# Kernel optimization log

Measured on AMD Instinct MI355X. Metric: run time of the kernel, lower is better.

The kernel has to match this reference:

```python
import jax, jax.numpy as jnp
import numpy as np

SUBSTEPS = 2  # fixed Tsit5 substeps per observation interval (replaces diffrax adaptive PID control)
# Tsit5 Butcher tableau (same stage math as diffrax.Tsit5)
C2, C3, C4, C5, C6 = 0.161, 0.327, 0.9, 0.9800255409045097, 1.0
A21 = 0.161
A31, A32 = -0.008480655492356989, 0.335480655492357
A41, A42, A43 = 2.8971530571054935, -6.359448489975075, 4.3622954328695815
A51, A52, A53, A54 = 5.325864828439257, -11.748883564062828, 7.4955393428898365, -0.09249506636175525
A61, A62, A63, A64, A65 = 5.86145544294642, -12.92096931784711, 8.159367898576159, -0.071584973281401, -0.028269050394068383
B1, B2, B3, B4, B5, B6 = 0.09646076681806523, 0.01, 0.4798896504144996, 1.379008574103742, -3.290069515436081, 2.324710524099774


def setup_inputs() -> dict:
    key = jax.random.key(0)
    ks = jax.random.split(key, 12)
    B, N, D_IN, H, ST, SW, OW, D_OUT = 128, 64, 32, 128, 16, 256, 256, 16

    def lin(k, o, i):
        return jax.random.normal(k, (o, i), jnp.float32) / np.sqrt(i).astype(np.float32)

    # strictly increasing timestamps with small intervals
    dts = jax.random.uniform(ks[0], (B, N), jnp.float32) * 0.05 + 0.01
    ts_batch = jnp.cumsum(dts, axis=1)
    X_batch = jax.random.normal(ks[1], (B, N, D_IN), jnp.float32)
    Static_batch = jax.random.normal(ks[2], (B, ST), jnp.float32)
    return dict(
        ts_batch=ts_batch, X_batch=X_batch, Static_batch=Static_batch,
        ode_w0=lin(ks[3], SW, 1 + H), ode_b0=jnp.zeros(SW, jnp.float32),
        ode_w1=lin(ks[4], SW, SW), ode_b1=jnp.zeros(SW, jnp.float32),
        ode_w2=lin(ks[5], H, SW), ode_b2=jnp.zeros(H, jnp.float32),
        ode_scale=jnp.array(1.0, jnp.float32),
        rnn_wh=lin(ks[6], H, H), rnn_wx=lin(ks[7], H, D_IN), rnn_bx=jnp.zeros(H, jnp.float32),
        inj_w=lin(ks[8], H, H + ST), inj_b=jnp.zeros(H, jnp.float32),
        out_w0=lin(ks[9], OW, H), out_b0=jnp.zeros(OW, jnp.float32),
        out_w1=lin(ks[10], OW, OW), out_b1=jnp.zeros(OW, jnp.float32),
        out_w2=lin(ks[11], D_OUT, OW), out_b2=jnp.zeros(D_OUT, jnp.float32),
    )


def reference(ts_batch, X_batch, Static_batch,
              ode_w0, ode_b0, ode_w1, ode_b1, ode_w2, ode_b2, ode_scale,
              rnn_wh, rnn_wx, rnn_bx, inj_w, inj_b,
              out_w0, out_b0, out_w1, out_b1, out_w2, out_b2):
    def f(t, h):  # vector field: t (B,), h (B,H)
        z = jnp.concatenate([t[:, None], h], axis=-1)
        z = jax.nn.silu(z @ ode_w0.T + ode_b0)
        z = jax.nn.silu(z @ ode_w1.T + ode_b1)
        return ode_scale * jnp.tanh(z @ ode_w2.T + ode_b2)

    def tsit5_step(t, dt, y):  # one Tsit5 step, batched over B
        d = dt[:, None]
        k1 = f(t, y)
        k2 = f(t + C2 * dt, y + d * (A21 * k1))
        k3 = f(t + C3 * dt, y + d * (A31 * k1 + A32 * k2))
        k4 = f(t + C4 * dt, y + d * (A41 * k1 + A42 * k2 + A43 * k3))
        k5 = f(t + C5 * dt, y + d * (A51 * k1 + A52 * k2 + A53 * k3 + A54 * k4))
        k6 = f(t + C6 * dt, y + d * (A61 * k1 + A62 * k2 + A63 * k3 + A64 * k4 + A65 * k5))
        return y + d * (B1 * k1 + B2 * k2 + B3 * k3 + B4 * k4 + B5 * k5 + B6 * k6)

    def ode_solve(t0, t1, y):  # fixed-substep Tsit5 integration from t0 to t1 (per-batch times)
        dt = (t1 - t0) / SUBSTEPS
        def body(yc, i):
            t = t0 + i.astype(t0.dtype) * dt
            return tsit5_step(t, dt, yc), None
        y, _ = jax.lax.scan(body, y, jnp.arange(SUBSTEPS))
        return y

    def rnn(h_prime, x):
        return jnp.tanh(h_prime @ rnn_wh.T + x @ rnn_wx.T + rnn_bx)

    # h0: rnn_cell(zeros, x0) -> inject static -> tanh
    h0 = jnp.tanh(X_batch[:, 0] @ rnn_wx.T + rnn_bx)  # hidden_linear(0) == 0
    h0 = jnp.tanh(jnp.concatenate([h0, Static_batch], axis=-1) @ inj_w.T + inj_b)

    xs = (ts_batch[:, :-1].T, ts_batch[:, 1:].T, jnp.swapaxes(X_batch[:, 1:], 0, 1))
    def step(h, inp):
        tp, tn, x = inp
        hp = ode_solve(tp, tn, h)
        return rnn(hp, x), None
    hN, _ = jax.lax.scan(step, h0, xs)

    z = jnp.tanh(hN @ out_w0.T + out_b0)
    z = jnp.tanh(z @ out_w1.T + out_b1)
    return z @ out_w2.T + out_b2  # (B, output_dim)
```

## Files before the change

### kernel.cpp

```cpp
#include <hip/hip_runtime.h>

typedef _Float16 f16;
typedef _Float16 f16x4 __attribute__((ext_vector_type(4)));
typedef _Float16 f16x8 __attribute__((ext_vector_type(8)));
typedef float f32x4 __attribute__((ext_vector_type(4)));

#define MFMA16(a, b, c) __builtin_amdgcn_mfma_f32_16x16x32_f16((a), (b), (c), 0, 0, 0)

#define A21f 0.161f
#define A31f (-0.008480655492356989f)
#define A32f 0.335480655492357f
#define A41f 2.8971530571054935f
#define A42f (-6.359448489975075f)
#define A43f 4.3622954328695815f
#define A51f 5.325864828439257f
#define A52f (-11.748883564062828f)
#define A53f 7.4955393428898365f
#define A54f (-0.09249506636175525f)
#define A61f 5.86145544294642f
#define A62f (-12.92096931784711f)
#define A63f 8.159367898576159f
#define A64f (-0.071584973281401f)
#define A65f (-0.028269050394068383f)
#define B1f 0.09646076681806523f
#define B2f 0.01f
#define B3f 0.4798896504144996f
#define B4f 1.379008574103742f
#define B5f (-3.290069515436081f)
#define B6f 2.324710524099774f
#define C2f 0.161f
#define C3f 0.327f
#define C4f 0.9f
#define C5f 0.9800255409045097f
#define C6f 1.0f

#define LDS_Y   0
#define LDS_Z1  4096
#define LDS_Z2  12288
#define LDS_X   20480
#define LDS_TS  21504
#define LDS_WH  25600
#define LDS_TOT 58368

__device__ __forceinline__ float tanh_fast(float x) {
  return 2.0f * __builtin_amdgcn_rcpf(1.0f + __expf(-2.0f * x)) - 1.0f;
}
__device__ __forceinline__ float siluf(float x) {
  return x * __builtin_amdgcn_rcpf(1.0f + __expf(-x));
}

__global__ __launch_bounds__(512, 2)
void ode_rnn_kernel(const float* __restrict__ ts, const float* __restrict__ Xg,
                    const float* __restrict__ Sg,
                    const float* __restrict__ w0g, const float* __restrict__ b0g,
                    const float* __restrict__ w1g, const float* __restrict__ b1g,
                    const float* __restrict__ w2g, const float* __restrict__ b2g,
                    const float* __restrict__ scaleg,
                    const float* __restrict__ whg, const float* __restrict__ wxg,
                    const float* __restrict__ bxg,
                    const float* __restrict__ injwg, const float* __restrict__ injbg,
                    const float* __restrict__ ow0g, const float* __restrict__ ob0g,
                    const float* __restrict__ ow1g, const float* __restrict__ ob1g,
                    const float* __restrict__ ow2g, const float* __restrict__ ob2g,
                    float* __restrict__ outg) {
  const int t  = threadIdx.x;
  const int w  = t >> 6;
  const int l  = t & 63;
  const int lr = l & 15;
  const int lg = l >> 4;
  const int rb = blockIdx.x * 16;
  const int c1 = w * 32;
  const int c3 = w * 16;

  __shared__ __align__(16) unsigned char lds[LDS_TOT];

  const int ard = l * 16;
  const int whrd = LDS_WH + lg * 2048 + w * 256 + lr * 16;
  const int awb = (lg >> 1) * 256 + lr * 16 + (lg & 1) * 8;

  for (int e = t; e < 16 * 64; e += 512) {
    *(float*)(lds + LDS_TS + e * 4) = ts[(size_t)(rb + (e >> 6)) * 64 + (e & 63)];
  }
  for (int e = t; e < 128 * 128; e += 512) {
    int c = e >> 7, kk = e & 127;
    *(f16*)(lds + LDS_WH + ((kk >> 3) * 128 + c) * 16 + (kk & 7) * 2) = (f16)whg[e];
  }
  {
    int r = t >> 5, d = t & 31;
    *(f16*)(lds + LDS_X + (d >> 3) * 256 + r * 16 + (d & 7) * 2) =
        (f16)Xg[(size_t)(rb + r) * 2048 + d];
  }
  if (t < 256) {
    int r = t >> 4, c = t & 15;
    *(f16*)(lds + LDS_Z1 + 4096 + (c >> 3) * 256 + r * 16 + (c & 7) * 2) =
        (f16)Sg[(size_t)(rb + r) * 16 + c];
    *(f16*)(lds + LDS_Z1 + 4608 + (c >> 3) * 256 + r * 16 + (c & 7) * 2) = (f16)0.0f;
  }

  f32x4 b0q[2], b1q[2];
  float w0c0[2][4];
  #pragma unroll
  for (int nt = 0; nt < 2; ++nt) {
    b0q[nt] = *(const f32x4*)(b0g + c1 + nt * 16 + lg * 4);
    b1q[nt] = *(const f32x4*)(b1g + c1 + nt * 16 + lg * 4);
    #pragma unroll
    for (int r = 0; r < 4; ++r)
      w0c0[nt][r] = w0g[(size_t)(c1 + nt * 16 + lg * 4 + r) * 129];
  }
  const f32x4 b2q = *(const f32x4*)(b2g + c3 + lg * 4);
  const f32x4 bxq = *(const f32x4*)(bxg + c3 + lg * 4);
  const float scalev = scaleg[0];

  auto ldfrag = [](const float* p) {
    f16x8 v;
    #pragma unroll
    for (int j = 0; j < 8; ++j) v[j] = (f16)p[j];
    return v;
  };

  f16x8 W0f[4][2];
  #pragma unroll
  for (int kt = 0; kt < 4; ++kt)
    #pragma unroll
    for (int nt = 0; nt < 2; ++nt)
      W0f[kt][nt] = ldfrag(w0g + (size_t)(c1 + nt * 16 + lr) * 129 + 1 + kt * 32 + lg * 8);

  f16x8 W1f[8][2];
  #pragma unroll
  for (int kt = 0; kt < 8; ++kt)
    #pragma unroll
    for (int nt = 0; nt < 2; ++nt)
      W1f[kt][nt] = ldfrag(w1g + (size_t)(c1 + nt * 16 + lr) * 256 + kt * 32 + lg * 8);

  f16x8 W2f[8];
  #pragma unroll
  for (int kt = 0; kt < 8; ++kt)
    W2f[kt] = ldfrag(w2g + (size_t)(c3 + lr) * 256 + kt * 32 + lg * 8);

  f16x8 WXf = ldfrag(wxg + (size_t)(c3 + lr) * 32 + lg * 8);

  __syncthreads();

  float y[4];
  float tpv, dvv;

  auto writeY = [&](const float* yv) {
    f16x4 p;
    #pragma unroll
    for (int r = 0; r < 4; ++r) p[r] = (f16)yv[r];
    *(f16x4*)(lds + LDS_Y + w * 512 + awb) = p;
  };

  {
    f16x8 xa = *(const f16x8*)(lds + LDS_X + ard);
    f32x4 acc = {};
    acc = MFMA16(WXf, xa, acc);
    f16x4 p;
    #pragma unroll
    for (int r = 0; r < 4; ++r) p[r] = (f16)tanh_fast(acc[r] + bxq[r]);
    *(f16x4*)(lds + LDS_Z1 + w * 512 + awb) = p;
  }
  __syncthreads();
  {
    f16x8 af[5];
    #pragma unroll
    for (int kt = 0; kt < 5; ++kt) af[kt] = *(const f16x8*)(lds + LDS_Z1 + ard + kt * 1024);
    f32x4 acc = {};
    #pragma unroll
    for (int kt = 0; kt < 5; ++kt) {
      f16x8 bf;
      #pragma unroll
      for (int j = 0; j < 8; ++j) {
        int k = kt * 32 + lg * 8 + j;
        bf[j] = (k < 144) ? (f16)injwg[(size_t)(c3 + lr) * 144 + k] : (f16)0.0f;
      }
      acc = MFMA16(bf, af[kt], acc);
    }
    const f32x4 ibq = *(const f32x4*)(injbg + c3 + lg * 4);
    #pragma unroll
    for (int r = 0; r < 4; ++r) y[r] = tanh_fast(acc[r] + ibq[r]);
  }
  writeY(y);
  __syncthreads();

  auto feval = [&](float sc, float* ko) {
    f16x8 af[8];
    #pragma unroll
    for (int kt = 0; kt < 4; ++kt) af[kt] = *(const f16x8*)(lds + LDS_Y + ard + kt * 1024);
    f32x4 a1[2] = {}, a1b[2] = {};
    __builtin_amdgcn_s_setprio(1);
    #pragma unroll
    for (int kt = 0; kt < 2; ++kt)
      #pragma unroll
      for (int nt = 0; nt < 2; ++nt) {
        a1[nt]  = MFMA16(W0f[kt][nt],     af[kt],     a1[nt]);
        a1b[nt] = MFMA16(W0f[kt + 2][nt], af[kt + 2], a1b[nt]);
      }
    __builtin_amdgcn_s_setprio(0);
    const float tr = tpv + sc * dvv;
    #pragma unroll
    for (int nt = 0; nt < 2; ++nt) {
      f16x4 p;
      #pragma unroll
      for (int r = 0; r < 4; ++r)
        p[r] = (f16)siluf(a1[nt][r] + a1b[nt][r] + tr * w0c0[nt][r] + b0q[nt][r]);
      *(f16x4*)(lds + LDS_Z1 + w * 1024 + nt * 512 + awb) = p;
    }
    __syncthreads();
    #pragma unroll
    for (int kt = 0; kt < 8; ++kt) af[kt] = *(const f16x8*)(lds + LDS_Z1 + ard + kt * 1024);
    f32x4 a2[2] = {}, a2b[2] = {};
    __builtin_amdgcn_s_setprio(1);
    #pragma unroll
    for (int kt = 0; kt < 4; ++kt)
      #pragma unroll
      for (int nt = 0; nt < 2; ++nt) {
        a2[nt]  = MFMA16(W1f[kt][nt],     af[kt],     a2[nt]);
        a2b[nt] = MFMA16(W1f[kt + 4][nt], af[kt + 4], a2b[nt]);
      }
    __builtin_amdgcn_s_setprio(0);
    #pragma unroll
    for (int nt = 0; nt < 2; ++nt) {
      f16x4 p;
      #pragma unroll
      for (int r = 0; r < 4; ++r)
        p[r] = (f16)siluf(a2[nt][r] + a2b[nt][r] + b1q[nt][r]);
      *(f16x4*)(lds + LDS_Z2 + w * 1024 + nt * 512 + awb) = p;
    }
    __syncthreads();
    #pragma unroll
    for (int kt = 0; kt < 8; ++kt) af[kt] = *(const f16x8*)(lds + LDS_Z2 + ard + kt * 1024);
    f32x4 a3 = {}, a3b = {}, a3c = {}, a3d = {};
    __builtin_amdgcn_s_setprio(1);
    #pragma unroll
    for (int kt = 0; kt < 2; ++kt) {
      a3  = MFMA16(W2f[kt],     af[kt],     a3);
      a3b = MFMA16(W2f[kt + 2], af[kt + 2], a3b);
      a3c = MFMA16(W2f[kt + 4], af[kt + 4], a3c);
      a3d = MFMA16(W2f[kt + 6], af[kt + 6], a3d);
    }
    __builtin_amdgcn_s_setprio(0);
    #pragma unroll
    for (int r = 0; r < 4; ++r)
      ko[r] = scalev * tanh_fast(((a3[r] + a3b[r]) + (a3c[r] + a3d[r])) + b2q[r]);
  };

  #pragma unroll 1
  for (int n = 0; n < 63; ++n) {
    {
      float tp = *(const float*)(lds + LDS_TS + (lr * 64 + n) * 4);
      float tn = *(const float*)(lds + LDS_TS + (lr * 64 + n + 1) * 4);
      tpv = tp;
      dvv = (tn - tp) * 0.5f;
    }
    {
      int r = t >> 5, d = t & 31;
      *(f16*)(lds + LDS_X + (d >> 3) * 256 + r * 16 + (d & 7) * 2) =
          (f16)Xg[(size_t)(rb + r) * 2048 + (size_t)(n + 1) * 32 + d];
    }

    #pragma unroll 1
    for (int s = 0; s < 2; ++s) {
      float k1v[4], k2v[4], k3v[4], k4v[4], k5v[4], k6v[4], yt[4];
      float sf = (float)s;
      feval(sf, k1v);
      #pragma unroll
      for (int i = 0; i < 4; ++i) yt[i] = y[i] + dvv * (A21f * k1v[i]);
      writeY(yt); __syncthreads();
      feval(sf + C2f, k2v);
      #pragma unroll
      for (int i = 0; i < 4; ++i) yt[i] = y[i] + dvv * (A31f * k1v[i] + A32f * k2v[i]);
      writeY(yt); __syncthreads();
      feval(sf + C3f, k3v);
      #pragma unroll
      for (int i = 0; i < 4; ++i) yt[i] = y[i] + dvv * (A41f * k1v[i] + A42f * k2v[i] + A43f * k3v[i]);
      writeY(yt); __syncthreads();
      feval(sf + C4f, k4v);
      #pragma unroll
      for (int i = 0; i < 4; ++i) yt[i] = y[i] + dvv * (A51f * k1v[i] + A52f * k2v[i] + A53f * k3v[i] + A54f * k4v[i]);
      writeY(yt); __syncthreads();
      feval(sf + C5f, k5v);
      #pragma unroll
      for (int i = 0; i < 4; ++i) yt[i] = y[i] + dvv * (A61f * k1v[i] + A62f * k2v[i] + A63f * k3v[i] + A64f * k4v[i] + A65f * k5v[i]);
      writeY(yt); __syncthreads();
      feval(sf + C6f, k6v);
      #pragma unroll
      for (int i = 0; i < 4; ++i)
        y[i] += dvv * (B1f * k1v[i] + B2f * k2v[i] + B3f * k3v[i] + B4f * k4v[i] + B5f * k5v[i] + B6f * k6v[i]);
      writeY(y); __syncthreads();
    }

    {
      f16x8 ha[4];
      #pragma unroll
      for (int kt = 0; kt < 4; ++kt) ha[kt] = *(const f16x8*)(lds + LDS_Y + ard + kt * 1024);
      f16x8 xa = *(const f16x8*)(lds + LDS_X + ard);
      f32x4 acc = {}, accb = {};
      __builtin_amdgcn_s_setprio(1);
      #pragma unroll
      for (int kt = 0; kt < 2; ++kt) {
        f16x8 bf  = *(const f16x8*)(lds + whrd + kt * 8192);
        f16x8 bf2 = *(const f16x8*)(lds + whrd + (kt + 2) * 8192);
        acc  = MFMA16(bf,  ha[kt],     acc);
        accb = MFMA16(bf2, ha[kt + 2], accb);
      }
      acc = MFMA16(WXf, xa, acc);
      __builtin_amdgcn_s_setprio(0);
      #pragma unroll
      for (int r = 0; r < 4; ++r) y[r] = tanh_fast(acc[r] + accb[r] + bxq[r]);
      writeY(y);
      __syncthreads();
    }
  }

  auto ldfrag2 = [](const float* p) {
    f16x8 v;
    #pragma unroll
    for (int j = 0; j < 8; ++j) v[j] = (f16)p[j];
    return v;
  };
  {
    f16x8 ha[4];
    #pragma unroll
    for (int kt = 0; kt < 4; ++kt) ha[kt] = *(const f16x8*)(lds + LDS_Y + ard + kt * 1024);
    f32x4 acc[2] = {};
    #pragma unroll
    for (int kt = 0; kt < 4; ++kt)
      #pragma unroll
      for (int nt = 0; nt < 2; ++nt) {
        f16x8 bf = ldfrag2(ow0g + (size_t)(c1 + nt * 16 + lr) * 128 + kt * 32 + lg * 8);
        acc[nt] = MFMA16(bf, ha[kt], acc[nt]);
      }
    #pragma unroll
    for (int nt = 0; nt < 2; ++nt) {
      const f32x4 bb = *(const f32x4*)(ob0g + c1 + nt * 16 + lg * 4);
      f16x4 p;
      #pragma unroll
      for (int r = 0; r < 4; ++r) p[r] = (f16)tanh_fast(acc[nt][r] + bb[r]);
      *(f16x4*)(lds + LDS_Z1 + w * 1024 + nt * 512 + awb) = p;
    }
  }
  __syncthreads();
  {
    f16x8 za[8];
    #pragma unroll
    for (int kt = 0; kt < 8; ++kt) za[kt] = *(const f16x8*)(lds + LDS_Z1 + ard + kt * 1024);
    f32x4 acc[2] = {};
    #pragma unroll
    for (int kt = 0; kt < 8; ++kt)
      #pragma unroll
      for (int nt = 0; nt < 2; ++nt) {
        f16x8 bf = ldfrag2(ow1g + (size_t)(c1 + nt * 16 + lr) * 256 + kt * 32 + lg * 8);
        acc[nt] = MFMA16(bf, za[kt], acc[nt]);
      }
    #pragma unroll
    for (int nt = 0; nt < 2; ++nt) {
      const f32x4 bb = *(const f32x4*)(ob1g + c1 + nt * 16 + lg * 4);
      f16x4 p;
      #pragma unroll
      for (int r = 0; r < 4; ++r) p[r] = (f16)tanh_fast(acc[nt][r] + bb[r]);
      *(f16x4*)(lds + LDS_Z2 + w * 1024 + nt * 512 + awb) = p;
    }
  }
  __syncthreads();
  if (w == 0) {
    f16x8 za[8];
    #pragma unroll
    for (int kt = 0; kt < 8; ++kt) za[kt] = *(const f16x8*)(lds + LDS_Z2 + ard + kt * 1024);
    f32x4 acc = {};
    #pragma unroll
    for (int kt = 0; kt < 8; ++kt) {
      f16x8 bf = ldfrag2(ow2g + (size_t)lr * 256 + kt * 32 + lg * 8);
      acc = MFMA16(bf, za[kt], acc);
    }
    const f32x4 bb = *(const f32x4*)(ob2g + lg * 4);
    f32x4 vout;
    #pragma unroll
    for (int r = 0; r < 4; ++r) vout[r] = acc[r] + bb[r];
    *(f32x4*)(outg + (size_t)(rb + lr) * 16 + lg * 4) = vout;
  }
}

extern "C" void kernel_launch(void* const* d_in, const int* in_sizes, int n_in,
                              void* d_out, int out_size, void* d_ws, size_t ws_size,
                              hipStream_t stream) {
  (void)in_sizes; (void)n_in; (void)d_ws; (void)ws_size; (void)out_size;
  ode_rnn_kernel<<<dim3(8), dim3(512), 0, stream>>>(
      (const float*)d_in[0],  (const float*)d_in[1],  (const float*)d_in[2],
      (const float*)d_in[3],  (const float*)d_in[4],  (const float*)d_in[5],
      (const float*)d_in[6],  (const float*)d_in[7],  (const float*)d_in[8],
      (const float*)d_in[9],  (const float*)d_in[10], (const float*)d_in[11],
      (const float*)d_in[12], (const float*)d_in[13], (const float*)d_in[14],
      (const float*)d_in[15], (const float*)d_in[16], (const float*)d_in[17],
      (const float*)d_in[18], (const float*)d_in[19], (const float*)d_in[20],
      (float*)d_out);
}
```

Measured before the change: 1.163 ms.

## Use LDS-only barriers, double-buffer X prefetch, packed f16 conversion, reorder MFMAs

Replaces __syncthreads in the hot ODE loop with a barrier that waits only on lgkmcnt, so the global load of the next X row is no longer drained at every barrier. X is now double-buffered in LDS, and the next row is loaded into a register one step ahead, then written after the substeps. The f16 packing uses cvt_pkrtz (round toward zero rather than round-to-nearest), which slightly changes numerics. MFMA accumulation order is restructured per output tile.

```diff
diff --git a/kernel.cpp b/kernel.cpp
--- a/kernel.cpp
+++ b/kernel.cpp
@@ -1,9 +1,9 @@
 #include <hip/hip_runtime.h>
 
 typedef _Float16 f16;
-typedef _Float16 f16x4 __attribute__((ext_vector_type(4)));
 typedef _Float16 f16x8 __attribute__((ext_vector_type(8)));
 typedef float f32x4 __attribute__((ext_vector_type(4)));
+typedef unsigned u32x2 __attribute__((ext_vector_type(2)));
 
 #define MFMA16(a, b, c) __builtin_amdgcn_mfma_f32_16x16x32_f16((a), (b), (c), 0, 0, 0)
 
@@ -37,16 +37,25 @@
 #define LDS_Y   0
 #define LDS_Z1  4096
 #define LDS_Z2  12288
-#define LDS_X   20480
-#define LDS_TS  21504
-#define LDS_WH  25600
-#define LDS_TOT 58368
+#define LDS_X0  20480
+#define LDS_X1  21504
+#define LDS_TS  22528
+#define LDS_WH  26624
+#define LDS_TOT 59392
 
 __device__ __forceinline__ float tanh_fast(float x) {
   return 2.0f * __builtin_amdgcn_rcpf(1.0f + __expf(-2.0f * x)) - 1.0f;
 }
 __device__ __forceinline__ float siluf(float x) {
   return x * __builtin_amdgcn_rcpf(1.0f + __expf(-x));
+}
+__device__ __forceinline__ unsigned pk2(float a, float b) {
+  return __builtin_bit_cast(unsigned, __builtin_amdgcn_cvt_pkrtz(a, b));
+}
+__device__ __forceinline__ void bar_lds() {
+  asm volatile("s_waitcnt lgkmcnt(0)" ::: "memory");
+  __builtin_amdgcn_s_barrier();
+  __builtin_amdgcn_sched_barrier(0);
 }
 
 __global__ __launch_bounds__(512, 2)
@@ -74,9 +83,11 @@
 
   __shared__ __align__(16) unsigned char lds[LDS_TOT];
 
-  const int ard = l * 16;
+  const int ard  = l * 16;
   const int whrd = LDS_WH + lg * 2048 + w * 256 + lr * 16;
-  const int awb = (lg >> 1) * 256 + lr * 16 + (lg & 1) * 8;
+  const int awb  = (lg >> 1) * 256 + lr * 16 + (lg & 1) * 8;
+  const int xr = t >> 5, xd = t & 31;
+  const int xso = (xd >> 3) * 256 + xr * 16 + (xd & 7) * 2;
 
   for (int e = t; e < 16 * 64; e += 512) {
     *(float*)(lds + LDS_TS + e * 4) = ts[(size_t)(rb + (e >> 6)) * 64 + (e & 63)];
@@ -86,9 +97,9 @@
     *(f16*)(lds + LDS_WH + ((kk >> 3) * 128 + c) * 16 + (kk & 7) * 2) = (f16)whg[e];
   }
   {
-    int r = t >> 5, d = t & 31;
-    *(f16*)(lds + LDS_X + (d >> 3) * 256 + r * 16 + (d & 7) * 2) =
-        (f16)Xg[(size_t)(rb + r) * 2048 + d];
+    size_t base = (size_t)(rb + xr) * 2048 + xd;
+    *(f16*)(lds + LDS_X0 + xso) = (f16)Xg[base];
+    *(f16*)(lds + LDS_X1 + xso) = (f16)Xg[base + 32];
   }
   if (t < 256) {
     int r = t >> 4, c = t & 15;
@@ -145,20 +156,17 @@
   float tpv, dvv;
 
   auto writeY = [&](const float* yv) {
-    f16x4 p;
-    #pragma unroll
-    for (int r = 0; r < 4; ++r) p[r] = (f16)yv[r];
-    *(f16x4*)(lds + LDS_Y + w * 512 + awb) = p;
+    u32x2 p = { pk2(yv[0], yv[1]), pk2(yv[2], yv[3]) };
+    *(u32x2*)(lds + LDS_Y + w * 512 + awb) = p;
   };
 
   {
-    f16x8 xa = *(const f16x8*)(lds + LDS_X + ard);
+    f16x8 xa = *(const f16x8*)(lds + LDS_X0 + ard);
     f32x4 acc = {};
     acc = MFMA16(WXf, xa, acc);
-    f16x4 p;
-    #pragma unroll
-    for (int r = 0; r < 4; ++r) p[r] = (f16)tanh_fast(acc[r] + bxq[r]);
-    *(f16x4*)(lds + LDS_Z1 + w * 512 + awb) = p;
+    u32x2 p = { pk2(tanh_fast(acc[0] + bxq[0]), tanh_fast(acc[1] + bxq[1])),
+                pk2(tanh_fast(acc[2] + bxq[2]), tanh_fast(acc[3] + bxq[3])) };
+    *(u32x2*)(lds + LDS_Z1 + w * 512 + awb) = p;
   }
   __syncthreads();
   {
@@ -187,47 +195,59 @@
     f16x8 af[8];
     #pragma unroll
     for (int kt = 0; kt < 4; ++kt) af[kt] = *(const f16x8*)(lds + LDS_Y + ard + kt * 1024);
-    f32x4 a1[2] = {}, a1b[2] = {};
+    f32x4 a10 = {}, a10b = {}, a11 = {}, a11b = {};
     __builtin_amdgcn_s_setprio(1);
-    #pragma unroll
-    for (int kt = 0; kt < 2; ++kt)
-      #pragma unroll
-      for (int nt = 0; nt < 2; ++nt) {
-        a1[nt]  = MFMA16(W0f[kt][nt],     af[kt],     a1[nt]);
-        a1b[nt] = MFMA16(W0f[kt + 2][nt], af[kt + 2], a1b[nt]);
-      }
+    a10  = MFMA16(W0f[0][0], af[0], a10);
+    a10b = MFMA16(W0f[2][0], af[2], a10b);
+    a10  = MFMA16(W0f[1][0], af[1], a10);
+    a10b = MFMA16(W0f[3][0], af[3], a10b);
+    a11  = MFMA16(W0f[0][1], af[0], a11);
+    a11b = MFMA16(W0f[2][1], af[2], a11b);
+    a11  = MFMA16(W0f[1][1], af[1], a11);
+    a11b = MFMA16(W0f[3][1], af[3], a11b);
     __builtin_amdgcn_s_setprio(0);
     const float tr = tpv + sc * dvv;
-    #pragma unroll
-    for (int nt = 0; nt < 2; ++nt) {
-      f16x4 p;
-      #pragma unroll
-      for (int r = 0; r < 4; ++r)
-        p[r] = (f16)siluf(a1[nt][r] + a1b[nt][r] + tr * w0c0[nt][r] + b0q[nt][r]);
-      *(f16x4*)(lds + LDS_Z1 + w * 1024 + nt * 512 + awb) = p;
-    }
-    __syncthreads();
+    {
+      u32x2 p = { pk2(siluf(a10[0] + a10b[0] + tr * w0c0[0][0] + b0q[0][0]),
+                      siluf(a10[1] + a10b[1] + tr * w0c0[0][1] + b0q[0][1])),
+                  pk2(siluf(a10[2] + a10b[2] + tr * w0c0[0][2] + b0q[0][2]),
+                      siluf(a10[3] + a10b[3] + tr * w0c0[0][3] + b0q[0][3])) };
+      *(u32x2*)(lds + LDS_Z1 + w * 1024 + awb) = p;
+      u32x2 q = { pk2(siluf(a11[0] + a11b[0] + tr * w0c0[1][0] + b0q[1][0]),
+                      siluf(a11[1] + a11b[1] + tr * w0c0[1][1] + b0q[1][1])),
+                  pk2(siluf(a11[2] + a11b[2] + tr * w0c0[1][2] + b0q[1][2]),
+                      siluf(a11[3] + a11b[3] + tr * w0c0[1][3] + b0q[1][3])) };
+      *(u32x2*)(lds + LDS_Z1 + w * 1024 + 512 + awb) = q;
+    }
+    bar_lds();
     #pragma unroll
     for (int kt = 0; kt < 8; ++kt) af[kt] = *(const f16x8*)(lds + LDS_Z1 + ard + kt * 1024);
-    f32x4 a2[2] = {}, a2b[2] = {};
+    f32x4 a20 = {}, a20b = {}, a21 = {}, a21b = {};
     __builtin_amdgcn_s_setprio(1);
     #pragma unroll
-    for (int kt = 0; kt < 4; ++kt)
-      #pragma unroll
-      for (int nt = 0; nt < 2; ++nt) {
-        a2[nt]  = MFMA16(W1f[kt][nt],     af[kt],     a2[nt]);
-        a2b[nt] = MFMA16(W1f[kt + 4][nt], af[kt + 4], a2b[nt]);
-      }
+    for (int kt = 0; kt < 4; ++kt) {
+      a20  = MFMA16(W1f[kt][0],     af[kt],     a20);
+      a20b = MFMA16(W1f[kt + 4][0], af[kt + 4], a20b);
+    }
+    #pragma unroll
+    for (int kt = 0; kt < 4; ++kt) {
+      a21  = MFMA16(W1f[kt][1],     af[kt],     a21);
+      a21b = MFMA16(W1f[kt + 4][1], af[kt + 4], a21b);
+    }
     __builtin_amdgcn_s_setprio(0);
-    #pragma unroll
-    for (int nt = 0; nt < 2; ++nt) {
-      f16x4 p;
-      #pragma unroll
-      for (int r = 0; r < 4; ++r)
-        p[r] = (f16)siluf(a2[nt][r] + a2b[nt][r] + b1q[nt][r]);
-      *(f16x4*)(lds + LDS_Z2 + w * 1024 + nt * 512 + awb) = p;
-    }
-    __syncthreads();
+    {
+      u32x2 p = { pk2(siluf(a20[0] + a20b[0] + b1q[0][0]),
+                      siluf(a20[1] + a20b[1] + b1q[0][1])),
+                  pk2(siluf(a20[2] + a20b[2] + b1q[0][2]),
+                      siluf(a20[3] + a20b[3] + b1q[0][3])) };
+      *(u32x2*)(lds + LDS_Z2 + w * 1024 + awb) = p;
+      u32x2 q = { pk2(siluf(a21[0] + a21b[0] + b1q[1][0]),
+                      siluf(a21[1] + a21b[1] + b1q[1][1])),
+                  pk2(siluf(a21[2] + a21b[2] + b1q[1][2]),
+                      siluf(a21[3] + a21b[3] + b1q[1][3])) };
+      *(u32x2*)(lds + LDS_Z2 + w * 1024 + 512 + awb) = q;
+    }
+    bar_lds();
     #pragma unroll
     for (int kt = 0; kt < 8; ++kt) af[kt] = *(const f16x8*)(lds + LDS_Z2 + ard + kt * 1024);
     f32x4 a3 = {}, a3b = {}, a3c = {}, a3d = {};
@@ -253,11 +273,8 @@
       tpv = tp;
       dvv = (tn - tp) * 0.5f;
     }
-    {
-      int r = t >> 5, d = t & 31;
-      *(f16*)(lds + LDS_X + (d >> 3) * 256 + r * 16 + (d & 7) * 2) =
-          (f16)Xg[(size_t)(rb + r) * 2048 + (size_t)(n + 1) * 32 + d];
-    }
+    int xcol = (n + 2 > 63) ? 63 : (n + 2);
+    float xf = Xg[(size_t)(rb + xr) * 2048 + (size_t)xcol * 32 + xd];
 
     #pragma unroll 1
     for (int s = 0; s < 2; ++s) {
@@ -266,35 +283,37 @@
       feval(sf, k1v);
       #pragma unroll
       for (int i = 0; i < 4; ++i) yt[i] = y[i] + dvv * (A21f * k1v[i]);
-      writeY(yt); __syncthreads();
+      writeY(yt); bar_lds();
       feval(sf + C2f, k2v);
       #pragma unroll
       for (int i = 0; i < 4; ++i) yt[i] = y[i] + dvv * (A31f * k1v[i] + A32f * k2v[i]);
-      writeY(yt); __syncthreads();
+      writeY(yt); bar_lds();
       feval(sf + C3f, k3v);
       #pragma unroll
       for (int i = 0; i < 4; ++i) yt[i] = y[i] + dvv * (A41f * k1v[i] + A42f * k2v[i] + A43f * k3v[i]);
-      writeY(yt); __syncthreads();
+      writeY(yt); bar_lds();
       feval(sf + C4f, k4v);
       #pragma unroll
       for (int i = 0; i < 4; ++i) yt[i] = y[i] + dvv * (A51f * k1v[i] + A52f * k2v[i] + A53f * k3v[i] + A54f * k4v[i]);
-      writeY(yt); __syncthreads();
+      writeY(yt); bar_lds();
       feval(sf + C5f, k5v);
       #pragma unroll
       for (int i = 0; i < 4; ++i) yt[i] = y[i] + dvv * (A61f * k1v[i] + A62f * k2v[i] + A63f * k3v[i] + A64f * k4v[i] + A65f * k5v[i]);
-      writeY(yt); __syncthreads();
+      writeY(yt); bar_lds();
       feval(sf + C6f, k6v);
       #pragma unroll
       for (int i = 0; i < 4; ++i)
         y[i] += dvv * (B1f * k1v[i] + B2f * k2v[i] + B3f * k3v[i] + B4f * k4v[i] + B5f * k5v[i] + B6f * k6v[i]);
-      writeY(y); __syncthreads();
-    }
+      writeY(y); bar_lds();
+    }
+
+    *(f16*)(lds + LDS_X0 + ((n & 1) << 10) + xso) = (f16)xf;
 
     {
       f16x8 ha[4];
       #pragma unroll
       for (int kt = 0; kt < 4; ++kt) ha[kt] = *(const f16x8*)(lds + LDS_Y + ard + kt * 1024);
-      f16x8 xa = *(const f16x8*)(lds + LDS_X + ard);
+      f16x8 xa = *(const f16x8*)(lds + LDS_X0 + (((n + 1) & 1) << 10) + ard);
       f32x4 acc = {}, accb = {};
       __builtin_amdgcn_s_setprio(1);
       #pragma unroll
@@ -309,7 +328,7 @@
       #pragma unroll
       for (int r = 0; r < 4; ++r) y[r] = tanh_fast(acc[r] + accb[r] + bxq[r]);
       writeY(y);
-      __syncthreads();
+      bar_lds();
     }
   }
 
@@ -334,10 +353,9 @@
     #pragma unroll
     for (int nt = 0; nt < 2; ++nt) {
       const f32x4 bb = *(const f32x4*)(ob0g + c1 + nt * 16 + lg * 4);
-      f16x4 p;
-      #pragma unroll
-      for (int r = 0; r < 4; ++r) p[r] = (f16)tanh_fast(acc[nt][r] + bb[r]);
-      *(f16x4*)(lds + LDS_Z1 + w * 1024 + nt * 512 + awb) = p;
+      u32x2 p = { pk2(tanh_fast(acc[nt][0] + bb[0]), tanh_fast(acc[nt][1] + bb[1])),
+                  pk2(tanh_fast(acc[nt][2] + bb[2]), tanh_fast(acc[nt][3] + bb[3])) };
+      *(u32x2*)(lds + LDS_Z1 + w * 1024 + nt * 512 + awb) = p;
     }
   }
   __syncthreads();
@@ -356,10 +374,9 @@
     #pragma unroll
     for (int nt = 0; nt < 2; ++nt) {
       const f32x4 bb = *(const f32x4*)(ob1g + c1 + nt * 16 + lg * 4);
-      f16x4 p;
-      #pragma unroll
-      for (int r = 0; r < 4; ++r) p[r] = (f16)tanh_fast(acc[nt][r] + bb[r]);
-      *(f16x4*)(lds + LDS_Z2 + w * 1024 + nt * 512 + awb) = p;
+      u32x2 p = { pk2(tanh_fast(acc[nt][0] + bb[0]), tanh_fast(acc[nt][1] + bb[1])),
+                  pk2(tanh_fast(acc[nt][2] + bb[2]), tanh_fast(acc[nt][3] + bb[3])) };
+      *(u32x2*)(lds + LDS_Z2 + w * 1024 + nt * 512 + awb) = p;
     }
   }
   __syncthreads();
```

New measurement: 1.220 ms. 1.05x slower.
